# Kernel optimization log

Hardware: AMD Instinct MI355X
Metric: run time of the kernel (lower is better)

Reference implementation:

```python
import jax, jax.numpy as jnp
import numpy as np

B, T, D, MP = 32, 256, 512, 20


def setup_inputs() -> dict:
    key = jax.random.key(0)
    k1, k2, k3 = jax.random.split(key, 3)
    reps_lt = jax.random.normal(k1, (B, T, D), dtype=jnp.float32)
    reps_rt = jax.random.normal(k2, (B, T, D), dtype=jnp.float32)
    kernel = jax.random.normal(k3, (1, 1, 1, MP, D), dtype=jnp.float32)
    return {"reps_lt": reps_lt, "reps_rt": reps_rt, "kernel": kernel}


def reference(reps_lt, reps_rt, kernel):
    # kernel: (1,1,1,m,d) -> (m,d)
    km = kernel.reshape(kernel.shape[-2], kernel.shape[-1])
    # scores[b,t,s,m] = sum_d lt[b,t,d] * km[m,d] * rt[b,s,d]
    # matches original broadcast-multiply + sum over d (cosine_norm=False path)
    scores = jnp.einsum('btd,md,bsd->btsm', reps_lt, km, reps_rt)
    match = jnp.tanh(scores)               # [b, t1, t2, m]
    return jnp.max(match, axis=2)          # max-pool over t2 -> [b, t1, m]
```

## Files before the change

kernel.cpp:

```cpp
#include <hip/hip_runtime.h>


constexpr int TT = 256;
constexpr int DD = 512;
constexpr int NM = 20;
constexpr int NB = 32;
constexpr int BM = 64;
constexpr int NT = 16;

typedef float f32x4 __attribute__((ext_vector_type(4)));
typedef int   i32x8 __attribute__((ext_vector_type(8)));

__device__ __forceinline__ unsigned pack_bf16(float lo, float hi) {
    unsigned ulo = __builtin_bit_cast(unsigned, lo);
    unsigned uhi = __builtin_bit_cast(unsigned, hi);
    return (ulo >> 16) | (uhi & 0xFFFF0000u);
}

__device__ __forceinline__ unsigned pk4_fp8(float a, float b, float c, float d) {
    unsigned r = __builtin_amdgcn_cvt_pk_fp8_f32(a, b, 0, false);
    return __builtin_amdgcn_cvt_pk_fp8_f32(c, d, r, true);
}

__device__ __forceinline__ float blo(unsigned u) { return __builtin_bit_cast(float, u << 16); }
__device__ __forceinline__ float bhi(unsigned u) { return __builtin_bit_cast(float, u); }

__global__ __launch_bounds__(256)
void cast_inputs(const float* __restrict__ lt, const float* __restrict__ rt,
                 unsigned short* __restrict__ ltb, unsigned char* __restrict__ rtf)
{
    const int half = (int)gridDim.x >> 1;
    if ((int)blockIdx.x < half) {
        size_t base = ((size_t)blockIdx.x * 256 + threadIdx.x) * 8;
        float4 a = *(const float4*)(lt + base);
        float4 b = *(const float4*)(lt + base + 4);
        uint4 w;
        w.x = pack_bf16(a.x, a.y);
        w.y = pack_bf16(a.z, a.w);
        w.z = pack_bf16(b.x, b.y);
        w.w = pack_bf16(b.z, b.w);
        *(uint4*)(ltb + base) = w;
    } else {
        size_t base = ((size_t)(blockIdx.x - half) * 256 + threadIdx.x) * 8;
        float4 a = *(const float4*)(rt + base);
        float4 b = *(const float4*)(rt + base + 4);
        uint2 o;
        o.x = pk4_fp8(a.x, a.y, a.z, a.w);
        o.y = pk4_fp8(b.x, b.y, b.z, b.w);
        *(uint2*)(rtf + base) = o;
    }
}

__global__ __launch_bounds__(256, 3)
void mp_match_mx(const unsigned short* __restrict__ ltb, const unsigned char* __restrict__ rtf,
                 const float* __restrict__ km, float* __restrict__ out)
{
    __shared__ __attribute__((aligned(16))) uint4 Ash[BM * 33];
    __shared__ __attribute__((aligned(16))) float maxbuf[4][BM];

    const int f  = blockIdx.x;
    const int c8 = f & 7;
    const int i  = f >> 3;
    const int b  = c8 + 8 * (i / 80);
    const int j  = i % 80;
    const int m  = j >> 2;
    const int t0 = (j & 3) * BM;

    const int tid  = threadIdx.x;
    const int w    = tid >> 6;
    const int lane = tid & 63;
    const int l15  = lane & 15;
    const int l4   = lane >> 4;
    const int ws   = w * 64;

    const unsigned short* ltB = ltb + ((size_t)b * TT + t0) * DD;
    const unsigned char*  rtB = rtf + (size_t)b * TT * DD;
    const float*          kmp = km  + (size_t)m * DD;

    const unsigned char* bBase = rtB + (size_t)(ws + l15) * DD + l4 * 32;
    auto loadBj = [&](int t, i32x8* dst) {
        const unsigned char* p = bBase + (size_t)(t & 3) * 16 * DD + (t >> 2) * 128;
        ((uint4*)dst)[0] = *(const uint4*)p;
        ((uint4*)dst)[1] = *(const uint4*)(p + 16);
    };

    i32x8 bv[4];
    loadBj(0, &bv[0]);
    loadBj(1, &bv[1]);

    {
        const int cc = tid & 31, r0 = (tid >> 5) * 8;
        const float4 kA = *(const float4*)(kmp + cc * 16);
        const float4 kB = *(const float4*)(kmp + cc * 16 + 4);
        const float4 kC = *(const float4*)(kmp + cc * 16 + 8);
        const float4 kD = *(const float4*)(kmp + cc * 16 + 12);
#pragma unroll
        for (int r = 0; r < 8; ++r) {
            const unsigned short* src = ltB + (size_t)(r0 + r) * DD + cc * 16;
            uint4 h0 = *(const uint4*)src;
            uint4 h1 = *(const uint4*)(src + 8);
            uint4 o;
            o.x = pk4_fp8(blo(h0.x) * kA.x, bhi(h0.x) * kA.y, blo(h0.y) * kA.z, bhi(h0.y) * kA.w);
            o.y = pk4_fp8(blo(h0.z) * kB.x, bhi(h0.z) * kB.y, blo(h0.w) * kB.z, bhi(h0.w) * kB.w);
            o.z = pk4_fp8(blo(h1.x) * kC.x, bhi(h1.x) * kC.y, blo(h1.y) * kC.z, bhi(h1.y) * kC.w);
            o.w = pk4_fp8(blo(h1.z) * kD.x, bhi(h1.z) * kD.y, blo(h1.w) * kD.z, bhi(h1.w) * kD.w);
            Ash[(r0 + r) * 33 + cc] = o;
        }
    }
    __syncthreads();

    loadBj(2, &bv[2]);

    auto loadA = [&](int kk, i32x8* dst) {
#pragma unroll
        for (int ii = 0; ii < 4; ++ii) {
            int base = (ii * 16 + l15) * 33 + kk * 8 + l4 * 2;
            ((uint4*)&dst[ii])[0] = Ash[base];
            ((uint4*)&dst[ii])[1] = Ash[base + 1];
        }
    };

    f32x4 acc[4][4] = {};
    i32x8 av[4];
    loadA(0, av);

#pragma unroll
    for (int t = 0; t < NT; ++t) {
        if (t + 3 < NT) loadBj(t + 3, &bv[(t + 3) & 3]);
        const int jj = t & 3;
#pragma unroll
        for (int ii = 0; ii < 4; ++ii)
            acc[ii][jj] = __builtin_amdgcn_mfma_scale_f32_16x16x128_f8f6f4(
                av[ii], bv[jj], acc[ii][jj], 0, 0, 0, 127, 0, 127);
        if (jj == 3 && t + 1 < NT)
            loadA((t >> 2) + 1, av);
    }

#pragma unroll
    for (int ii = 0; ii < 4; ++ii) {
        f32x4 v = acc[ii][0];
#pragma unroll
        for (int jj = 1; jj < 4; ++jj) {
            v.x = fmaxf(v.x, acc[ii][jj].x);
            v.y = fmaxf(v.y, acc[ii][jj].y);
            v.z = fmaxf(v.z, acc[ii][jj].z);
            v.w = fmaxf(v.w, acc[ii][jj].w);
        }
#pragma unroll
        for (int off = 1; off < 16; off <<= 1) {
            v.x = fmaxf(v.x, __shfl_xor(v.x, off, 64));
            v.y = fmaxf(v.y, __shfl_xor(v.y, off, 64));
            v.z = fmaxf(v.z, __shfl_xor(v.z, off, 64));
            v.w = fmaxf(v.w, __shfl_xor(v.w, off, 64));
        }
        if (l15 == 0)
            *(f32x4*)&maxbuf[w][ii * 16 + l4 * 4] = v;
    }
    __syncthreads();
    if (tid < BM) {
        float v = fmaxf(fmaxf(maxbuf[0][tid], maxbuf[1][tid]),
                        fmaxf(maxbuf[2][tid], maxbuf[3][tid]));
        out[((size_t)b * TT + t0 + tid) * NM + m] = tanhf(v);
    }
}

typedef short bf16x8 __attribute__((ext_vector_type(8)));

__global__ __launch_bounds__(256, 2)
void mp_match_kernel(const float* __restrict__ lt, const float* __restrict__ rt,
                     const float* __restrict__ km, float* __restrict__ out)
{
    __shared__ __attribute__((aligned(16))) unsigned short Ash[2][4][128][8];
    __shared__ __attribute__((aligned(16))) unsigned short Bsh2[2][4][256][8];
    __shared__ __attribute__((aligned(16))) float maxbuf[2][128];

    const int ttile = blockIdx.x, m = blockIdx.y, b = blockIdx.z;
    const int t0 = ttile * 128;
    const int tid = threadIdx.x, wave = tid >> 6, lane = tid & 63;
    const int l15 = lane & 15, l4 = lane >> 4;
    const int wt = (wave & 1) * 64, wsi = wave >> 1;

    const float* ltp = lt + ((size_t)b * TT + t0) * DD;
    const float* rtp = rt + (size_t)b * TT * DD;
    const float* kmp = km + (size_t)m * DD;
    const int a_t = tid >> 1, a_h = tid & 1;

    f32x4 acc[4][8] = {};

    auto stage = [&](int kk, int buf) {
        const int d0 = kk * 32;
        const float* ap = ltp + (size_t)a_t * DD + d0 + a_h * 16;
        const float* kp = kmp + d0 + a_h * 16;
#pragma unroll
        for (int q = 0; q < 2; ++q) {
            float4 x0 = *(const float4*)(ap + q * 8);
            float4 x1 = *(const float4*)(ap + q * 8 + 4);
            float4 k0 = *(const float4*)(kp + q * 8);
            float4 k1 = *(const float4*)(kp + q * 8 + 4);
            uint4 wv;
            wv.x = pack_bf16(x0.x * k0.x, x0.y * k0.y);
            wv.y = pack_bf16(x0.z * k0.z, x0.w * k0.w);
            wv.z = pack_bf16(x1.x * k1.x, x1.y * k1.y);
            wv.w = pack_bf16(x1.z * k1.z, x1.w * k1.w);
            *(uint4*)&Ash[buf][a_h * 2 + q][a_t][0] = wv;
        }
        const float* bp = rtp + (size_t)tid * DD + d0;
#pragma unroll
        for (int p = 0; p < 4; ++p) {
            float4 y0 = *(const float4*)(bp + p * 8);
            float4 y1 = *(const float4*)(bp + p * 8 + 4);
            uint4 wv;
            wv.x = pack_bf16(y0.x, y0.y);
            wv.y = pack_bf16(y0.z, y0.w);
            wv.z = pack_bf16(y1.x, y1.y);
            wv.w = pack_bf16(y1.z, y1.w);
            *(uint4*)&Bsh2[buf][p][tid][0] = wv;
        }
    };

    stage(0, 0);
    for (int kk = 0; kk < 16; ++kk) {
        const int buf = kk & 1;
        __syncthreads();
        bf16x8 af[4], bfv[8];
#pragma unroll
        for (int i2 = 0; i2 < 4; ++i2)
            af[i2] = *(const bf16x8*)&Ash[buf][l4][wt + i2 * 16 + l15][0];
#pragma unroll
        for (int j2 = 0; j2 < 8; ++j2)
            bfv[j2] = *(const bf16x8*)&Bsh2[buf][l4][wsi * 128 + j2 * 16 + l15][0];
        if (kk + 1 < 16) stage(kk + 1, buf ^ 1);
#pragma unroll
        for (int i2 = 0; i2 < 4; ++i2)
#pragma unroll
            for (int j2 = 0; j2 < 8; ++j2)
                acc[i2][j2] = __builtin_amdgcn_mfma_f32_16x16x32_bf16(af[i2], bfv[j2], acc[i2][j2], 0, 0, 0);
    }
#pragma unroll
    for (int i2 = 0; i2 < 4; ++i2) {
        f32x4 v = acc[i2][0];
#pragma unroll
        for (int j2 = 1; j2 < 8; ++j2) {
            v.x = fmaxf(v.x, acc[i2][j2].x); v.y = fmaxf(v.y, acc[i2][j2].y);
            v.z = fmaxf(v.z, acc[i2][j2].z); v.w = fmaxf(v.w, acc[i2][j2].w);
        }
#pragma unroll
        for (int off = 1; off < 16; off <<= 1) {
            v.x = fmaxf(v.x, __shfl_xor(v.x, off, 64));
            v.y = fmaxf(v.y, __shfl_xor(v.y, off, 64));
            v.z = fmaxf(v.z, __shfl_xor(v.z, off, 64));
            v.w = fmaxf(v.w, __shfl_xor(v.w, off, 64));
        }
        if (l15 == 0) *(f32x4*)&maxbuf[wsi][wt + i2 * 16 + l4 * 4] = v;
    }
    __syncthreads();
    if (tid < 128) {
        float v = fmaxf(maxbuf[0][tid], maxbuf[1][tid]);
        out[((size_t)b * TT + t0 + tid) * NM + m] = tanhf(v);
    }
}

extern "C" void kernel_launch(void* const* d_in, const int* in_sizes, int n_in,
                              void* d_out, int out_size, void* d_ws, size_t ws_size,
                              hipStream_t stream) {
    const float* lt  = (const float*)d_in[0];
    const float* rt  = (const float*)d_in[1];
    const float* km  = (const float*)d_in[2];
    float*       out = (float*)d_out;

    const size_t elems = (size_t)NB * TT * DD;
    const size_t ltbB  = elems * sizeof(unsigned short);
    const size_t rtfB  = elems;

    if (ws_size >= ltbB + rtfB) {
        unsigned short* ltb = (unsigned short*)d_ws;
        unsigned char*  rtf = (unsigned char*)((char*)d_ws + ltbB);
        cast_inputs<<<4096, 256, 0, stream>>>(lt, rt, ltb, rtf);
        mp_match_mx<<<2560, 256, 0, stream>>>(ltb, rtf, km, out);
    } else {
        mp_match_kernel<<<dim3(2, NM, NB), 256, 0, stream>>>(lt, rt, km, out);
    }
}
```

Before: 124.2 us.

## Split t2 across blocks, stage B via async LDS loads, add combine kernel

Each block now covers half of the s (t2) range for a 64-row t tile, which doubles the grid to 5120 blocks. The rt tile is staged into double-buffered, XOR-swizzled LDS using global_load_lds async copies instead of per-lane register loads. The A tile uses the same swizzle in place of padding. Partial maxima are written to workspace and a new combine kernel takes the max of the two halves and applies tanh. This aims for more parallelism and overlapped, bank-conflict-free B loads, at the cost of an extra launch, extra global traffic, 64KB LDS per block and lower occupancy (2 blocks).

```diff
diff --git a/kernel.cpp b/kernel.cpp
--- a/kernel.cpp
+++ b/kernel.cpp
@@ -5,11 +5,16 @@
 constexpr int DD = 512;
 constexpr int NM = 20;
 constexpr int NB = 32;
-constexpr int BM = 64;
-constexpr int NT = 16;
+constexpr int NKS = 4;
 
 typedef float f32x4 __attribute__((ext_vector_type(4)));
 typedef int   i32x8 __attribute__((ext_vector_type(8)));
+
+__device__ __forceinline__ void async_ld16(const void* g, void* l) {
+    __builtin_amdgcn_global_load_lds(
+        (const __attribute__((address_space(1))) void*)g,
+        (__attribute__((address_space(3))) void*)l, 16, 0, 0);
+}
 
 __device__ __forceinline__ unsigned pack_bf16(float lo, float hi) {
     unsigned ulo = __builtin_bit_cast(unsigned, lo);
@@ -51,101 +56,115 @@
     }
 }
 
-__global__ __launch_bounds__(256, 3)
+__global__ __launch_bounds__(256, 2)
 void mp_match_mx(const unsigned short* __restrict__ ltb, const unsigned char* __restrict__ rtf,
-                 const float* __restrict__ km, float* __restrict__ out)
+                 const float* __restrict__ km, float* __restrict__ part)
 {
-    __shared__ __attribute__((aligned(16))) uint4 Ash[BM * 33];
-    __shared__ __attribute__((aligned(16))) float maxbuf[4][BM];
+    __shared__ __attribute__((aligned(16))) char pool[65536];
+    uint4* Ash  = (uint4*)pool;
+    uint4* Bsh0 = (uint4*)(pool + 32768);
+    uint4* Bsh1 = (uint4*)(pool + 49152);
+    float* maxbuf = (float*)pool;
 
     const int f  = blockIdx.x;
     const int c8 = f & 7;
     const int i  = f >> 3;
-    const int b  = c8 + 8 * (i / 80);
-    const int j  = i % 80;
-    const int m  = j >> 2;
-    const int t0 = (j & 3) * BM;
+    const int b  = c8 + 8 * (i / 160);
+    const int j  = i % 160;
+    const int m  = j >> 3;
+    const int r3 = j & 7;
+    const int t0 = (r3 >> 1) * 64;
+    const int sT = r3 & 1;
+    const int s0 = sT * 128;
 
     const int tid  = threadIdx.x;
     const int w    = tid >> 6;
     const int lane = tid & 63;
     const int l15  = lane & 15;
     const int l4   = lane >> 4;
-    const int ws   = w * 64;
+    const int ws   = w * 32;
 
     const unsigned short* ltB = ltb + ((size_t)b * TT + t0) * DD;
-    const unsigned char*  rtB = rtf + (size_t)b * TT * DD;
+    const unsigned char*  rtB = rtf + ((size_t)b * TT + s0) * DD;
     const float*          kmp = km  + (size_t)m * DD;
 
-    const unsigned char* bBase = rtB + (size_t)(ws + l15) * DD + l4 * 32;
-    auto loadBj = [&](int t, i32x8* dst) {
-        const unsigned char* p = bBase + (size_t)(t & 3) * 16 * DD + (t >> 2) * 128;
-        ((uint4*)dst)[0] = *(const uint4*)p;
-        ((uint4*)dst)[1] = *(const uint4*)(p + 16);
+    auto issueB = [&](int kk, uint4* buf) {
+#pragma unroll
+        for (int q = 0; q < 4; ++q) {
+            int slot = q * 256 + tid;
+            int row  = slot >> 3;
+            int cg   = (slot & 7) ^ (row & 7);
+            async_ld16(rtB + (size_t)row * DD + kk * 128 + cg * 16,
+                       (char*)buf + (size_t)slot * 16);
+        }
     };
 
-    i32x8 bv[4];
-    loadBj(0, &bv[0]);
-    loadBj(1, &bv[1]);
-
+    const int cc = tid & 31, r0 = (tid >> 5) * 8;
+    uint4 h[8][2];
     {
-        const int cc = tid & 31, r0 = (tid >> 5) * 8;
-        const float4 kA = *(const float4*)(kmp + cc * 16);
-        const float4 kB = *(const float4*)(kmp + cc * 16 + 4);
-        const float4 kC = *(const float4*)(kmp + cc * 16 + 8);
-        const float4 kD = *(const float4*)(kmp + cc * 16 + 12);
-#pragma unroll
-        for (int r = 0; r < 8; ++r) {
-            const unsigned short* src = ltB + (size_t)(r0 + r) * DD + cc * 16;
-            uint4 h0 = *(const uint4*)src;
-            uint4 h1 = *(const uint4*)(src + 8);
-            uint4 o;
-            o.x = pk4_fp8(blo(h0.x) * kA.x, bhi(h0.x) * kA.y, blo(h0.y) * kA.z, bhi(h0.y) * kA.w);
-            o.y = pk4_fp8(blo(h0.z) * kB.x, bhi(h0.z) * kB.y, blo(h0.w) * kB.z, bhi(h0.w) * kB.w);
-            o.z = pk4_fp8(blo(h1.x) * kC.x, bhi(h1.x) * kC.y, blo(h1.y) * kC.z, bhi(h1.y) * kC.w);
-            o.w = pk4_fp8(blo(h1.z) * kD.x, bhi(h1.z) * kD.y, blo(h1.w) * kD.z, bhi(h1.w) * kD.w);
-            Ash[(r0 + r) * 33 + cc] = o;
-        }
-    }
+        const unsigned short* src0 = ltB + cc * 16;
+#pragma unroll
+        for (int rr = 0; rr < 8; ++rr) {
+            const unsigned short* s = src0 + (size_t)(r0 + rr) * DD;
+            h[rr][0] = *(const uint4*)s;
+            h[rr][1] = *(const uint4*)(s + 8);
+        }
+    }
+    const float4 kA = *(const float4*)(kmp + cc * 16);
+    const float4 kB = *(const float4*)(kmp + cc * 16 + 4);
+    const float4 kC = *(const float4*)(kmp + cc * 16 + 8);
+    const float4 kD = *(const float4*)(kmp + cc * 16 + 12);
+    issueB(0, Bsh0);
+#pragma unroll
+    for (int rr = 0; rr < 8; ++rr) {
+        uint4 h0 = h[rr][0], h1 = h[rr][1];
+        uint4 o;
+        o.x = pk4_fp8(blo(h0.x) * kA.x, bhi(h0.x) * kA.y, blo(h0.y) * kA.z, bhi(h0.y) * kA.w);
+        o.y = pk4_fp8(blo(h0.z) * kB.x, bhi(h0.z) * kB.y, blo(h0.w) * kB.z, bhi(h0.w) * kB.w);
+        o.z = pk4_fp8(blo(h1.x) * kC.x, bhi(h1.x) * kC.y, blo(h1.y) * kC.z, bhi(h1.y) * kC.w);
+        o.w = pk4_fp8(blo(h1.z) * kD.x, bhi(h1.z) * kD.y, blo(h1.w) * kD.z, bhi(h1.w) * kD.w);
+        const int row = r0 + rr;
+        Ash[row * 32 + (cc & ~7) + ((cc & 7) ^ (row & 7))] = o;
+    }
+
+    f32x4 acc[4][2] = {};
+
+#pragma unroll
+    for (int kk = 0; kk < NKS; ++kk) {
+        __syncthreads();
+        if (kk + 1 < NKS) issueB(kk + 1, (kk & 1) ? Bsh0 : Bsh1);
+        const uint4* Bc = (kk & 1) ? Bsh1 : Bsh0;
+        i32x8 av[4], bv[2];
+#pragma unroll
+        for (int ii = 0; ii < 4; ++ii) {
+            const int row = ii * 16 + l15;
+            const int base = row * 32 + kk * 8;
+            ((uint4*)&av[ii])[0] = Ash[base + ((2 * l4)     ^ (row & 7))];
+            ((uint4*)&av[ii])[1] = Ash[base + ((2 * l4 + 1) ^ (row & 7))];
+        }
+#pragma unroll
+        for (int jj = 0; jj < 2; ++jj) {
+            const int row = ws + jj * 16 + l15;
+            ((uint4*)&bv[jj])[0] = Bc[row * 8 + ((2 * l4)     ^ (row & 7))];
+            ((uint4*)&bv[jj])[1] = Bc[row * 8 + ((2 * l4 + 1) ^ (row & 7))];
+        }
+#pragma unroll
+        for (int ii = 0; ii < 4; ++ii)
+#pragma unroll
+            for (int jj = 0; jj < 2; ++jj)
+                acc[ii][jj] = __builtin_amdgcn_mfma_scale_f32_16x16x128_f8f6f4(
+                    av[ii], bv[jj], acc[ii][jj], 0, 0, 0, 127, 0, 127);
+    }
+
     __syncthreads();
-
-    loadBj(2, &bv[2]);
-
-    auto loadA = [&](int kk, i32x8* dst) {
-#pragma unroll
-        for (int ii = 0; ii < 4; ++ii) {
-            int base = (ii * 16 + l15) * 33 + kk * 8 + l4 * 2;
-            ((uint4*)&dst[ii])[0] = Ash[base];
-            ((uint4*)&dst[ii])[1] = Ash[base + 1];
-        }
-    };
-
-    f32x4 acc[4][4] = {};
-    i32x8 av[4];
-    loadA(0, av);
-
-#pragma unroll
-    for (int t = 0; t < NT; ++t) {
-        if (t + 3 < NT) loadBj(t + 3, &bv[(t + 3) & 3]);
-        const int jj = t & 3;
-#pragma unroll
-        for (int ii = 0; ii < 4; ++ii)
-            acc[ii][jj] = __builtin_amdgcn_mfma_scale_f32_16x16x128_f8f6f4(
-                av[ii], bv[jj], acc[ii][jj], 0, 0, 0, 127, 0, 127);
-        if (jj == 3 && t + 1 < NT)
-            loadA((t >> 2) + 1, av);
-    }
 
 #pragma unroll
     for (int ii = 0; ii < 4; ++ii) {
         f32x4 v = acc[ii][0];
-#pragma unroll
-        for (int jj = 1; jj < 4; ++jj) {
-            v.x = fmaxf(v.x, acc[ii][jj].x);
-            v.y = fmaxf(v.y, acc[ii][jj].y);
-            v.z = fmaxf(v.z, acc[ii][jj].z);
-            v.w = fmaxf(v.w, acc[ii][jj].w);
-        }
+        v.x = fmaxf(v.x, acc[ii][1].x);
+        v.y = fmaxf(v.y, acc[ii][1].y);
+        v.z = fmaxf(v.z, acc[ii][1].z);
+        v.w = fmaxf(v.w, acc[ii][1].w);
 #pragma unroll
         for (int off = 1; off < 16; off <<= 1) {
             v.x = fmaxf(v.x, __shfl_xor(v.x, off, 64));
@@ -154,14 +173,22 @@
             v.w = fmaxf(v.w, __shfl_xor(v.w, off, 64));
         }
         if (l15 == 0)
-            *(f32x4*)&maxbuf[w][ii * 16 + l4 * 4] = v;
+            *(f32x4*)&maxbuf[w * 64 + ii * 16 + l4 * 4] = v;
     }
     __syncthreads();
-    if (tid < BM) {
-        float v = fmaxf(fmaxf(maxbuf[0][tid], maxbuf[1][tid]),
-                        fmaxf(maxbuf[2][tid], maxbuf[3][tid]));
-        out[((size_t)b * TT + t0 + tid) * NM + m] = tanhf(v);
-    }
+    if (tid < 64) {
+        float v = fmaxf(fmaxf(maxbuf[tid], maxbuf[64 + tid]),
+                        fmaxf(maxbuf[128 + tid], maxbuf[192 + tid]));
+        part[(((size_t)sT * NB + b) * TT + t0 + tid) * NM + m] = v;
+    }
+}
+
+__global__ __launch_bounds__(256)
+void mp_combine(const float* __restrict__ part, float* __restrict__ out, int n)
+{
+    int idx = blockIdx.x * 256 + threadIdx.x;
+    if (idx < n)
+        out[idx] = tanhf(fmaxf(part[idx], part[(size_t)n + idx]));
 }
 
 typedef short bf16x8 __attribute__((ext_vector_type(8)));
@@ -271,12 +298,16 @@
     const size_t elems = (size_t)NB * TT * DD;
     const size_t ltbB  = elems * sizeof(unsigned short);
     const size_t rtfB  = elems;
-
-    if (ws_size >= ltbB + rtfB) {
+    const int    nOut  = NB * TT * NM;
+    const size_t partB = 2 * (size_t)nOut * sizeof(float);
+
+    if (ws_size >= ltbB + rtfB + partB) {
         unsigned short* ltb = (unsigned short*)d_ws;
         unsigned char*  rtf = (unsigned char*)((char*)d_ws + ltbB);
+        float* part = (float*)((char*)d_ws + ltbB + rtfB);
         cast_inputs<<<4096, 256, 0, stream>>>(lt, rt, ltb, rtf);
-        mp_match_mx<<<2560, 256, 0, stream>>>(ltb, rtf, km, out);
+        mp_match_mx<<<5120, 256, 0, stream>>>(ltb, rtf, km, part);
+        mp_combine<<<(nOut + 255) / 256, 256, 0, stream>>>(part, out, nOut);
     } else {
         mp_match_kernel<<<dim3(2, NM, NB), 256, 0, stream>>>(lt, rt, km, out);
     }
```

Measured after the change: 141.0 us. 13.6% more time.
